# Performance work log

Measured on AMD Instinct MI355X. Metric: run time of the kernel, lower is better.

The kernel has to match this reference:

```python
import jax, jax.numpy as jnp
import numpy as np

WINDOW_SIZE = 128

def setup_inputs() -> dict:
    key = jax.random.key(0)
    kq, kk, kv = jax.random.split(key, 3)
    B, S, D = 4, 4096, 128
    q = jax.random.normal(kq, (B, S, D), dtype=jnp.float32)
    k = jax.random.normal(kk, (B, S, D), dtype=jnp.float32)
    v = jax.random.normal(kv, (B, S, D), dtype=jnp.float32)
    return {"q": q, "k": k, "v": v}

def reference(q, k, v):
    B, S, D = q.shape
    q = q / jnp.sqrt(jnp.asarray(D, q.dtype))
    # band mask: tril(window_size-1) & triu(-(window_size-1)) == |i - j| <= window_size-1
    i = jax.lax.broadcasted_iota(jnp.int32, (S, S), 0)
    j = jax.lax.broadcasted_iota(jnp.int32, (S, S), 1)
    mask = jnp.abs(i - j) <= (WINDOW_SIZE - 1)
    scores = jnp.einsum('bqd,bkd->bqk', q, k)  # [B,S,S]
    scores = jnp.where(mask, scores, jnp.asarray(-1e9, scores.dtype))
    weights = jax.nn.softmax(scores, axis=-1)
    return jnp.einsum('bqk,bkd->bqd', weights, v)
```

## Files before the change

kernel.cpp:

```cpp
#include <hip/hip_runtime.h>


typedef __attribute__((ext_vector_type(8))) _Float16 half8;
typedef __attribute__((ext_vector_type(2))) __fp16 fp16x2;
typedef __attribute__((ext_vector_type(4))) float floatx4;

#define MFMA_F16(a, b, c) __builtin_amdgcn_mfma_f32_16x16x32_f16(a, b, c, 0, 0, 0)

constexpr int S_ = 4096, D_ = 128, W_ = 127;
constexpr int BQ = 64, BK = 64;
constexpr int PST = 72;
constexpr int OST = 132;

union SMem {
  struct {
    _Float16 Kh[2][BK * D_];
    _Float16 Vt[2][D_ * BK];
    _Float16 Ps[4][16 * PST];
  } a;
  struct {
    float Om[4][16 * OST];
  } b;
};

__device__ __forceinline__ unsigned pk2(float a, float b) {
  union { fp16x2 h; unsigned u; } c;
  c.h = __builtin_amdgcn_cvt_pkrtz(a, b);
  return c.u;
}

__device__ __forceinline__ void gll16(const _Float16* g, _Float16* l) {
  __builtin_amdgcn_global_load_lds(
      (const __attribute__((address_space(1))) void*)g,
      (__attribute__((address_space(3))) void*)l, 16, 0, 0);
}

__global__ __launch_bounds__(256, 4)
void prep_kernel(const float* __restrict__ kg, const float* __restrict__ vg,
                 _Float16* __restrict__ K16, _Float16* __restrict__ Vt16)
{
  __shared__ __align__(16) _Float16 Vs[BK * D_];
  const int t  = threadIdx.x;
  const int bb = blockIdx.x >> 6;
  const int c  = blockIdx.x & 63;
  const size_t base = ((size_t)bb * S_ + c * 64) * D_;

#pragma unroll
  for (int j = 0; j < 4; ++j) {
    const int id = t + 256 * j;
    const int s = id >> 4, blk = id & 15;
    const float* src = kg + base + s * D_ + blk * 8;
    float4 a  = *(const float4*)src;
    float4 b2 = *(const float4*)(src + 4);
    uint4 w;
    w.x = pk2(a.x, a.y);  w.y = pk2(a.z, a.w);
    w.z = pk2(b2.x, b2.y); w.w = pk2(b2.z, b2.w);
    *(uint4*)(K16 + base + s * D_ + 8 * (blk ^ (s & 7))) = w;
  }

  const int vr = t >> 5, vc = t & 31;
  float4 vf[8];
#pragma unroll
  for (int u = 0; u < 8; ++u)
    vf[u] = *(const float4*)(vg + base + (8 * vr + u) * D_ + 4 * vc);
#pragma unroll
  for (int i = 0; i < 4; ++i) {
    uint4 tv;
    tv.x = pk2(((const float*)&vf[0])[i], ((const float*)&vf[1])[i]);
    tv.y = pk2(((const float*)&vf[2])[i], ((const float*)&vf[3])[i]);
    tv.z = pk2(((const float*)&vf[4])[i], ((const float*)&vf[5])[i]);
    tv.w = pk2(((const float*)&vf[6])[i], ((const float*)&vf[7])[i]);
    const int d = 4 * vc + i;
    *(uint4*)(&Vs[d * 64 + 8 * (vr ^ (d & 7))]) = tv;
  }
  __syncthreads();
  _Float16* vdst = Vt16 + (size_t)(bb * 64 + c) * (D_ * 64);
#pragma unroll
  for (int i = 0; i < 4; ++i) {
    const int id2 = t + 256 * i;
    *(uint4*)(vdst + id2 * 8) = *(const uint4*)(&Vs[id2 * 8]);
  }
}

__global__ __launch_bounds__(256, 2)
void swa_v7_kernel(const float* __restrict__ qg,
                   const _Float16* __restrict__ K16,
                   const _Float16* __restrict__ Vt16,
                   float* __restrict__ og)
{
  __shared__ __align__(16) SMem sm;
  const int tid  = threadIdx.x;
  const int lane = tid & 63;
  const int wave = tid >> 6;
  const int lx   = lane & 15;
  const int quad = lane >> 4;

  const int bid = blockIdx.x;
  const int lid = (bid & 7) * 32 + (bid >> 3);
  const int bb  = lid >> 6;
  const int q0  = (lid & 63) * BQ;

  const float* qb = qg + (size_t)bb * S_ * D_;
  float*       ob = og + (size_t)bb * S_ * D_;

  const int qrow = q0 + 16 * wave + lx;
  half8 qh[4], ql[4];
#pragma unroll
  for (int ks = 0; ks < 4; ++ks) {
    const float* p = qb + (size_t)qrow * D_ + 32 * ks + 8 * quad;
#pragma unroll
    for (int j = 0; j < 8; ++j) {
      float f = p[j];
      _Float16 h = (_Float16)f;
      qh[ks][j] = h;
      ql[ks][j] = (_Float16)(f - (float)h);
    }
  }

  floatx4 o[8];
#pragma unroll
  for (int dt = 0; dt < 8; ++dt) o[dt] = (floatx4){0.f, 0.f, 0.f, 0.f};
  float lp[4] = {0.f, 0.f, 0.f, 0.f};

  const int kstart = (q0 > W_) ? (q0 - W_) : 0;
  int kend = q0 + BQ - 1 + W_;
  if (kend > S_ - 1) kend = S_ - 1;
  const int c0 = kstart >> 6, c1 = kend >> 6;

  const int ilo = q0 + 16 * wave, ihi = ilo + 15;
  const float C1 = 0.12751727f, C2 = -5.7707802f;

  const int sh  = wave >> 1;
  const int sub = wave & 1;

  {
    const int b0 = c0 & 1;
    const _Float16* kcb = K16 + ((size_t)bb * S_ + c0 * 64) * D_;
    const _Float16* vcb = Vt16 + (size_t)(bb * 64 + c0) * (D_ * 64);
#pragma unroll
    for (int i = 0; i < 8; ++i) {
      const int ofs = (sub * 8 + i) * 512;
      if (sh == 0) gll16(kcb + ofs + lane * 8, &sm.a.Kh[b0][ofs]);
      else         gll16(vcb + ofs + lane * 8, &sm.a.Vt[b0][ofs]);
    }
  }

  for (int c = c0; c <= c1; ++c) {
    const int buf = c & 1;
    asm volatile("s_waitcnt vmcnt(0)" ::: "memory");
    __builtin_amdgcn_s_barrier();
    asm volatile("" ::: "memory");

    if (c < c1) {
      const _Float16* kcb = K16 + ((size_t)bb * S_ + (c + 1) * 64) * D_;
      const _Float16* vcb = Vt16 + (size_t)(bb * 64 + (c + 1)) * (D_ * 64);
#pragma unroll
      for (int i = 0; i < 8; ++i) {
        const int ofs = (sub * 8 + i) * 512;
        if (sh == 0) gll16(kcb + ofs + lane * 8, &sm.a.Kh[buf ^ 1][ofs]);
        else         gll16(vcb + ofs + lane * 8, &sm.a.Vt[buf ^ 1][ofs]);
      }
    }

    const int kc = c * BK;
    if (kc + BK - 1 < ilo - W_ || kc > ihi + W_) continue;

    floatx4 acc[4];
#pragma unroll
    for (int ct = 0; ct < 4; ++ct) acc[ct] = (floatx4){0.f, 0.f, 0.f, 0.f};
#pragma unroll
    for (int ks = 0; ks < 4; ++ks) {
#pragma unroll
      for (int ct = 0; ct < 4; ++ct) {
        const int row = 16 * ct + lx;
        half8 bfr = *(const half8*)(
            &sm.a.Kh[buf][row * D_ + 8 * ((4 * ks + quad) ^ (lx & 7))]);
        acc[ct] = MFMA_F16(qh[ks], bfr, acc[ct]);
        acc[ct] = MFMA_F16(ql[ks], bfr, acc[ct]);
      }
    }

    const int ibase = q0 + 16 * wave + 4 * quad;
#pragma unroll
    for (int r = 0; r < 4; ++r) {
      const int i = ibase + r;
      float psum = 0.f;
#pragma unroll
      for (int ct = 0; ct < 4; ++ct) {
        const int col = kc + 16 * ct + lx;
        const bool v = (unsigned)(col - i + W_) <= (unsigned)(2 * W_);
        const float e = __builtin_amdgcn_exp2f(__builtin_fmaf(acc[ct][r], C1, C2));
        const float p = v ? e : 0.f;
        psum += p;
        sm.a.Ps[wave][(4 * quad + r) * PST + 16 * ct + lx] = (_Float16)p;
      }
      lp[r] += psum;
    }
    asm volatile("s_waitcnt lgkmcnt(0)" ::: "memory");
    half8 pa0 = *(const half8*)(&sm.a.Ps[wave][lx * PST + 8 * quad]);
    half8 pa1 = *(const half8*)(&sm.a.Ps[wave][lx * PST + 32 + 8 * quad]);

#pragma unroll
    for (int dt = 0; dt < 8; ++dt) {
      const int d = 16 * dt + lx;
      half8 v0 = *(const half8*)(&sm.a.Vt[buf][d * 64 + 8 * (quad ^ (d & 7))]);
      half8 v1 = *(const half8*)(&sm.a.Vt[buf][d * 64 + 8 * ((4 + quad) ^ (d & 7))]);
      o[dt] = MFMA_F16(pa0, v0, o[dt]);
      o[dt] = MFMA_F16(pa1, v1, o[dt]);
    }
  }

  float inv[4];
#pragma unroll
  for (int r = 0; r < 4; ++r) {
    float s = lp[r];
    s += __shfl_xor(s, 1);
    s += __shfl_xor(s, 2);
    s += __shfl_xor(s, 4);
    s += __shfl_xor(s, 8);
    inv[r] = 1.f / s;
  }

  __syncthreads();
#pragma unroll
  for (int dt = 0; dt < 8; ++dt)
#pragma unroll
    for (int r = 0; r < 4; ++r)
      sm.b.Om[wave][(4 * quad + r) * OST + 16 * dt + lx] = o[dt][r] * inv[r];
  __syncthreads();

  const int row = tid >> 2, seg = tid & 3;
  const int tl = row >> 4, r16 = row & 15;
  const float* src = &sm.b.Om[tl][r16 * OST + 32 * seg];
  float* dst = ob + (size_t)(q0 + row) * D_ + 32 * seg;
#pragma unroll
  for (int t = 0; t < 8; ++t)
    *(float4*)(dst + 4 * t) = *(const float4*)(src + 4 * t);
}

extern "C" void kernel_launch(void* const* d_in, const int* in_sizes, int n_in,
                              void* d_out, int out_size, void* d_ws, size_t ws_size,
                              hipStream_t stream) {
  const float* q = (const float*)d_in[0];
  const float* k = (const float*)d_in[1];
  const float* v = (const float*)d_in[2];
  float* out = (float*)d_out;

  const int B = in_sizes[0] / (S_ * D_);
  _Float16* K16  = (_Float16*)d_ws;
  _Float16* Vt16 = (_Float16*)d_ws + (size_t)B * S_ * D_;

  prep_kernel<<<dim3(B * (S_ / BK)), dim3(256), 0, stream>>>(k, v, K16, Vt16);
  swa_v7_kernel<<<dim3(B * (S_ / BQ)), dim3(256), 0, stream>>>(q, K16, Vt16, out);
}
```

Before: 89.44 us.

## Use 128-wide key tiles, single-buffer loads, and drop split-precision Q MFMA

Key/value tiles grow from 64 to 128 columns, so each query block walks fewer chunks. Double-buffered prefetch is replaced by a synchronous load with a barrier at the end of every iteration. The hi/lo fp16 split of Q is dropped, which halves the QK MFMAs. The per-wave band-skip check is removed, and launch bounds drop to one block per SIMD. This trades less loop overhead and fewer MFMAs for exposed load latency, lower occupancy and reduced QK accuracy.

New measurement: 92.19 us. 1.03x slower.

```diff
diff --git a/kernel.cpp b/kernel.cpp
--- a/kernel.cpp
+++ b/kernel.cpp
@@ -8,14 +8,14 @@
 #define MFMA_F16(a, b, c) __builtin_amdgcn_mfma_f32_16x16x32_f16(a, b, c, 0, 0, 0)
 
 constexpr int S_ = 4096, D_ = 128, W_ = 127;
-constexpr int BQ = 64, BK = 64;
-constexpr int PST = 72;
+constexpr int BQ = 64, BK = 128;
+constexpr int PST = 136;
 constexpr int OST = 132;
 
 union SMem {
   struct {
-    _Float16 Kh[2][BK * D_];
-    _Float16 Vt[2][D_ * BK];
+    _Float16 Kh[BK * D_];
+    _Float16 Vs[2 * 64 * D_];
     _Float16 Ps[4][16 * PST];
   } a;
   struct {
@@ -39,7 +39,7 @@
 void prep_kernel(const float* __restrict__ kg, const float* __restrict__ vg,
                  _Float16* __restrict__ K16, _Float16* __restrict__ Vt16)
 {
-  __shared__ __align__(16) _Float16 Vs[BK * D_];
+  __shared__ __align__(16) _Float16 Vsh[64 * D_];
   const int t  = threadIdx.x;
   const int bb = blockIdx.x >> 6;
   const int c  = blockIdx.x & 63;
@@ -71,19 +71,19 @@
     tv.z = pk2(((const float*)&vf[4])[i], ((const float*)&vf[5])[i]);
     tv.w = pk2(((const float*)&vf[6])[i], ((const float*)&vf[7])[i]);
     const int d = 4 * vc + i;
-    *(uint4*)(&Vs[d * 64 + 8 * (vr ^ (d & 7))]) = tv;
+    *(uint4*)(&Vsh[d * 64 + 8 * (vr ^ (d & 7))]) = tv;
   }
   __syncthreads();
   _Float16* vdst = Vt16 + (size_t)(bb * 64 + c) * (D_ * 64);
 #pragma unroll
   for (int i = 0; i < 4; ++i) {
     const int id2 = t + 256 * i;
-    *(uint4*)(vdst + id2 * 8) = *(const uint4*)(&Vs[id2 * 8]);
-  }
-}
-
-__global__ __launch_bounds__(256, 2)
-void swa_v7_kernel(const float* __restrict__ qg,
+    *(uint4*)(vdst + id2 * 8) = *(const uint4*)(&Vsh[id2 * 8]);
+  }
+}
+
+__global__ __launch_bounds__(256, 1)
+void swa_v9_kernel(const float* __restrict__ qg,
                    const _Float16* __restrict__ K16,
                    const _Float16* __restrict__ Vt16,
                    float* __restrict__ og)
@@ -102,19 +102,16 @@
 
   const float* qb = qg + (size_t)bb * S_ * D_;
   float*       ob = og + (size_t)bb * S_ * D_;
+  const _Float16* Kb = K16 + (size_t)bb * S_ * D_;
+  const _Float16* Vb = Vt16 + (size_t)bb * 64 * (D_ * 64);
 
   const int qrow = q0 + 16 * wave + lx;
-  half8 qh[4], ql[4];
+  half8 qh[4];
 #pragma unroll
   for (int ks = 0; ks < 4; ++ks) {
     const float* p = qb + (size_t)qrow * D_ + 32 * ks + 8 * quad;
 #pragma unroll
-    for (int j = 0; j < 8; ++j) {
-      float f = p[j];
-      _Float16 h = (_Float16)f;
-      qh[ks][j] = h;
-      ql[ks][j] = (_Float16)(f - (float)h);
-    }
+    for (int j = 0; j < 8; ++j) qh[ks][j] = (_Float16)p[j];
   }
 
   floatx4 o[8];
@@ -122,71 +119,55 @@
   for (int dt = 0; dt < 8; ++dt) o[dt] = (floatx4){0.f, 0.f, 0.f, 0.f};
   float lp[4] = {0.f, 0.f, 0.f, 0.f};
 
+  const int ilo = q0 + 16 * wave, ihi = ilo + 15;
   const int kstart = (q0 > W_) ? (q0 - W_) : 0;
   int kend = q0 + BQ - 1 + W_;
   if (kend > S_ - 1) kend = S_ - 1;
-  const int c0 = kstart >> 6, c1 = kend >> 6;
-
-  const int ilo = q0 + 16 * wave, ihi = ilo + 15;
+  const int c0 = kstart >> 7, c1 = kend >> 7;
+
   const float C1 = 0.12751727f, C2 = -5.7707802f;
 
-  const int sh  = wave >> 1;
-  const int sub = wave & 1;
-
-  {
-    const int b0 = c0 & 1;
-    const _Float16* kcb = K16 + ((size_t)bb * S_ + c0 * 64) * D_;
-    const _Float16* vcb = Vt16 + (size_t)(bb * 64 + c0) * (D_ * 64);
-#pragma unroll
-    for (int i = 0; i < 8; ++i) {
-      const int ofs = (sub * 8 + i) * 512;
-      if (sh == 0) gll16(kcb + ofs + lane * 8, &sm.a.Kh[b0][ofs]);
-      else         gll16(vcb + ofs + lane * 8, &sm.a.Vt[b0][ofs]);
-    }
-  }
-
   for (int c = c0; c <= c1; ++c) {
-    const int buf = c & 1;
+    if (wave < 2) {
+      const _Float16* kcb = Kb + (size_t)c * BK * D_;
+#pragma unroll
+      for (int i = 0; i < 16; ++i) {
+        const int seg = (wave * 16 + i) * 512;
+        gll16(kcb + seg + lane * 8, &sm.a.Kh[seg]);
+      }
+    } else {
+      const _Float16* vcb = Vb + (size_t)(2 * c) * (64 * D_);
+#pragma unroll
+      for (int i = 0; i < 16; ++i) {
+        const int seg = ((wave - 2) * 16 + i) * 512;
+        gll16(vcb + seg + lane * 8, &sm.a.Vs[seg]);
+      }
+    }
     asm volatile("s_waitcnt vmcnt(0)" ::: "memory");
     __builtin_amdgcn_s_barrier();
     asm volatile("" ::: "memory");
 
-    if (c < c1) {
-      const _Float16* kcb = K16 + ((size_t)bb * S_ + (c + 1) * 64) * D_;
-      const _Float16* vcb = Vt16 + (size_t)(bb * 64 + (c + 1)) * (D_ * 64);
-#pragma unroll
-      for (int i = 0; i < 8; ++i) {
-        const int ofs = (sub * 8 + i) * 512;
-        if (sh == 0) gll16(kcb + ofs + lane * 8, &sm.a.Kh[buf ^ 1][ofs]);
-        else         gll16(vcb + ofs + lane * 8, &sm.a.Vt[buf ^ 1][ofs]);
+    floatx4 acc[8];
+#pragma unroll
+    for (int ct = 0; ct < 8; ++ct) acc[ct] = (floatx4){0.f, 0.f, 0.f, 0.f};
+#pragma unroll
+    for (int ks = 0; ks < 4; ++ks) {
+      const int blk = 8 * ((4 * ks + quad) ^ (lx & 7));
+#pragma unroll
+      for (int ct = 0; ct < 8; ++ct) {
+        half8 bfr = *(const half8*)(&sm.a.Kh[(16 * ct + lx) * D_ + blk]);
+        acc[ct] = MFMA_F16(qh[ks], bfr, acc[ct]);
       }
     }
 
     const int kc = c * BK;
-    if (kc + BK - 1 < ilo - W_ || kc > ihi + W_) continue;
-
-    floatx4 acc[4];
-#pragma unroll
-    for (int ct = 0; ct < 4; ++ct) acc[ct] = (floatx4){0.f, 0.f, 0.f, 0.f};
-#pragma unroll
-    for (int ks = 0; ks < 4; ++ks) {
-#pragma unroll
-      for (int ct = 0; ct < 4; ++ct) {
-        const int row = 16 * ct + lx;
-        half8 bfr = *(const half8*)(
-            &sm.a.Kh[buf][row * D_ + 8 * ((4 * ks + quad) ^ (lx & 7))]);
-        acc[ct] = MFMA_F16(qh[ks], bfr, acc[ct]);
-        acc[ct] = MFMA_F16(ql[ks], bfr, acc[ct]);
-      }
-    }
-
     const int ibase = q0 + 16 * wave + 4 * quad;
 #pragma unroll
     for (int r = 0; r < 4; ++r) {
       const int i = ibase + r;
       float psum = 0.f;
 #pragma unroll
-      for (int ct = 0; ct < 4; ++ct) {
+      for (int ct = 0; ct < 8; ++ct) {
         const int col = kc + 16 * ct + lx;
         const bool v = (unsigned)(col - i + W_) <= (unsigned)(2 * W_);
         const float e = __builtin_amdgcn_exp2f(__builtin_fmaf(acc[ct][r], C1, C2));
@@ -197,17 +178,24 @@
       lp[r] += psum;
     }
     asm volatile("s_waitcnt lgkmcnt(0)" ::: "memory");
-    half8 pa0 = *(const half8*)(&sm.a.Ps[wave][lx * PST + 8 * quad]);
-    half8 pa1 = *(const half8*)(&sm.a.Ps[wave][lx * PST + 32 + 8 * quad]);
+    half8 pa[4];
+#pragma unroll
+    for (int kq = 0; kq < 4; ++kq)
+      pa[kq] = *(const half8*)(&sm.a.Ps[wave][lx * PST + 32 * kq + 8 * quad]);
 
 #pragma unroll
     for (int dt = 0; dt < 8; ++dt) {
       const int d = 16 * dt + lx;
-      half8 v0 = *(const half8*)(&sm.a.Vt[buf][d * 64 + 8 * (quad ^ (d & 7))]);
-      half8 v1 = *(const half8*)(&sm.a.Vt[buf][d * 64 + 8 * ((4 + quad) ^ (d & 7))]);
-      o[dt] = MFMA_F16(pa0, v0, o[dt]);
-      o[dt] = MFMA_F16(pa1, v1, o[dt]);
-    }
+#pragma unroll
+      for (int kq = 0; kq < 4; ++kq) {
+        const int h = kq >> 1;
+        const int kb = 4 * (kq & 1) + quad;
+        half8 vfr = *(const half8*)(
+            &sm.a.Vs[h * (64 * D_) + d * 64 + 8 * (kb ^ (d & 7))]);
+        o[dt] = MFMA_F16(pa[kq], vfr, o[dt]);
+      }
+    }
+    __syncthreads();
   }
 
   float inv[4];
@@ -221,7 +209,6 @@
     inv[r] = 1.f / s;
   }
 
-  __syncthreads();
 #pragma unroll
   for (int dt = 0; dt < 8; ++dt)
 #pragma unroll
@@ -250,6 +237,6 @@
   _Float16* K16  = (_Float16*)d_ws;
   _Float16* Vt16 = (_Float16*)d_ws + (size_t)B * S_ * D_;
 
-  prep_kernel<<<dim3(B * (S_ / BK)), dim3(256), 0, stream>>>(k, v, K16, Vt16);
-  swa_v7_kernel<<<dim3(B * (S_ / BQ)), dim3(256), 0, stream>>>(q, K16, Vt16, out);
-}
+  prep_kernel<<<dim3(B * 64), dim3(256), 0, stream>>>(k, v, K16, Vt16);
+  swa_v9_kernel<<<dim3(B * (S_ / BQ)), dim3(256), 0, stream>>>(q, K16, Vt16, out);
+}
```
